# Kernel tuning notes

Measured on AMD Instinct MI355X. Metric: run time of the kernel, lower is better.

## Reference

```python
import jax, jax.numpy as jnp
import numpy as np

B, L, D_MODEL, EXPAND, HEADDIM, QK_DIM = 2, 512, 512, 2, 128, 16
D_INNER = EXPAND * D_MODEL            # 1024
NHEADS = D_INNER // HEADDIM           # 8
EPS = 1e-3
STD_DEV = 1.0 / np.sqrt(2 * L * QK_DIM)
TWO_PI = 2.0 * np.pi


def setup_inputs() -> dict:
    key = jax.random.key(0)
    kv, kq, kk = jax.random.split(key, 3)
    v = jax.random.normal(kv, (B, L, D_INNER), dtype=jnp.float32)
    q = jax.random.normal(kq, (B, L, NHEADS * QK_DIM), dtype=jnp.float32)
    k = jax.random.normal(kk, (B, L, NHEADS * QK_DIM), dtype=jnp.float32)
    return {"v": v, "q": q, "k": k}


def reference(v, q, k):
    b, l, dim = v.shape
    residual = v
    # b l (n h) -> b l n h
    vh = v.reshape(b, l, NHEADS, HEADDIM)
    # b l (n d) -> b n d l
    qh = q.reshape(b, l, NHEADS, QK_DIM).transpose(0, 2, 3, 1)
    kh = k.reshape(b, l, NHEADS, QK_DIM).transpose(0, 2, 3, 1)
    pos = jnp.arange(l, dtype=v.dtype)  # position indices
    c = jnp.asarray(TWO_PI * EPS, dtype=v.dtype)
    # q_matrix[b,n,d,t,l] = cos(c * q[b,n,d,t] * pos[l])
    q_mat = jnp.cos(c * qh[:, :, :, :, None] * pos)
    # k_matrix[b,n,d,l,t] = cos(c * k[b,n,d,t] * pos[l])
    k_mat = jnp.cos(c * kh[:, :, :, None, :] * pos[:, None])
    sym = (q_mat - k_mat).sum(axis=2)  # (b, n, t, l)
    out = jnp.einsum('bntl,blnh->btnh', sym, vh)
    out = jnp.asarray(STD_DEV, v.dtype) * out
    return out.reshape(b, l, dim) + residual
```

## Files before the change

kernel.cpp:

```cpp
#include <hip/hip_runtime.h>

#define L_SEQ   512
#define NHEADS_ 8
#define HEADDIM_ 128
#define QKD     16
#define DINNER  1024
#define EPS_F   1e-3f
#define STD_F   0.0078125f

#define KS_ROW  529

typedef __attribute__((ext_vector_type(8))) short  short8;
typedef __attribute__((ext_vector_type(4))) float  floatx4;
typedef __attribute__((ext_vector_type(2))) float  float2v;

__device__ __forceinline__ float cosrev(float rev) {
    float r = rev - floorf(rev);
    return __builtin_amdgcn_cosf(r);
}

__device__ __forceinline__ float two_cos_small(float a) {
    float x = a * a;
    return fmaf(fmaf(x, 129.8787876f, -39.4784176f), x, 2.0f);
}

__device__ __forceinline__ unsigned short f2bf_rne(float x) {
    union { float f; unsigned int u; } v;
    v.f = x;
    unsigned int r = v.u + 0x7fffu + ((v.u >> 16) & 1u);
    return (unsigned short)(r >> 16);
}

__device__ __forceinline__ short8 pack_bf16x8(const float* s) {
    union { int i[4]; short8 v; } u;
#pragma unroll
    for (int p = 0; p < 4; ++p)
        asm("v_cvt_pk_bf16_f32 %0, %1, %2"
            : "=v"(u.i[p]) : "v"(s[2 * p]), "v"(s[2 * p + 1]));
    return u.v;
}

__device__ __forceinline__ float tree8(const float2v* C) {
    float2v s = ((C[0] + C[1]) + (C[2] + C[3])) + ((C[4] + C[5]) + (C[6] + C[7]));
    return s.x + s.y;
}

__global__ __launch_bounds__(256) void vtrans_kernel(const float* __restrict__ v,
                                                     unsigned short* __restrict__ vt) {
    const int bid = blockIdx.x;
    const int tid = threadIdx.x;
    const int l0 = (bid & 7) * 64;
    const int h0 = ((bid >> 3) & 1) * 64;
    const int bn = bid >> 4;
    const int b = bn >> 3, n = bn & 7;
    __shared__ float tile[64][65];
    const float* vb = v + ((size_t)b * L_SEQ) * DINNER + n * HEADDIM_;
    float4 r[4];
#pragma unroll
    for (int i = 0; i < 4; ++i) {
        int f = i * 256 + tid;
        int hq = f & 15, ll = f >> 4;
        r[i] = *(const float4*)(vb + (size_t)(l0 + ll) * DINNER + (h0 + hq * 4));
    }
#pragma unroll
    for (int i = 0; i < 4; ++i) {
        int f = i * 256 + tid;
        int hq = f & 15, ll = f >> 4;
        tile[hq * 4 + 0][ll] = r[i].x;
        tile[hq * 4 + 1][ll] = r[i].y;
        tile[hq * 4 + 2][ll] = r[i].z;
        tile[hq * 4 + 3][ll] = r[i].w;
    }
    __syncthreads();
    unsigned short* vdst = vt + (size_t)bn * (64 * 128 * 8);
#pragma unroll
    for (int i = 0; i < 2; ++i) {
        int f = i * 256 + tid;
        int hh = f & 63;
        int lc = f >> 6;
        short8 pk;
#pragma unroll
        for (int j = 0; j < 8; ++j)
            pk[j] = (short)f2bf_rne(tile[hh][lc * 8 + j]);
        *(short8*)(vdst + ((size_t)((l0 >> 3) + lc) * 128 + (h0 + hh)) * 8) = pk;
    }
}

__global__ __launch_bounds__(256, 2) void vand_fused(const float* __restrict__ v,
                                                     const float* __restrict__ q,
                                                     const float* __restrict__ k,
                                                     const unsigned short* __restrict__ vt,
                                                     float* __restrict__ out) {
    const int tid  = threadIdx.x;
    const int w    = tid >> 6;
    const int lane = tid & 63;
    const int tl   = lane & 15;
    const int quad = lane >> 4;
    const int ttile = blockIdx.x;
    const int bn    = blockIdx.y;
    const int b = bn >> 3, n = bn & 7;
    const float t0f = (float)(ttile * 16);

    __shared__ float smem[16 * KS_ROW];
    float* ksl = smem;

    float4 kf[2][4];
#pragma unroll
    for (int rep = 0; rep < 2; ++rep) {
        const int l = w * 128 + rep * 64 + lane;
        const float* krow = k + ((size_t)(b * L_SEQ + l)) * (NHEADS_ * QKD) + n * QKD;
#pragma unroll
        for (int d4 = 0; d4 < 4; ++d4)
            kf[rep][d4] = *(const float4*)(krow + 4 * d4);
    }
    const int t = ttile * 16 + tl;
    const float* qrow = q + ((size_t)(b * L_SEQ + t)) * (NHEADS_ * QKD) + n * QKD;
    float4 qf[4];
#pragma unroll
    for (int d4 = 0; d4 < 4; ++d4)
        qf[d4] = *(const float4*)(qrow + 4 * d4);
    const float* vbase = v + ((size_t)b * L_SEQ) * DINNER + n * HEADDIM_;
    float4 vres[2];
    size_t gis[2];
#pragma unroll
    for (int i = 0; i < 2; ++i) {
        int g    = i * 256 + tid;
        int hb   = g & 31;
        int tloc = g >> 5;
        gis[i] = (size_t)(ttile * 16 + tloc) * DINNER + hb * 4;
        vres[i] = *(const float4*)(vbase + gis[i]);
    }

#pragma unroll
    for (int rep = 0; rep < 2; ++rep) {
        const int l = w * 128 + rep * 64 + lane;
        float kk[16];
#pragma unroll
        for (int d4 = 0; d4 < 4; ++d4) {
            kk[d4 * 4 + 0] = kf[rep][d4].x; kk[d4 * 4 + 1] = kf[rep][d4].y;
            kk[d4 * 4 + 2] = kf[rep][d4].z; kk[d4 * 4 + 3] = kf[rep][d4].w;
        }
        float2v M2[8], X[8], Y[8];
#pragma unroll
        for (int i = 0; i < 8; ++i) {
            float a0 = EPS_F * kk[2 * i], a1 = EPS_F * kk[2 * i + 1];
            M2[i].x = two_cos_small(a0);        M2[i].y = two_cos_small(a1);
            Y[i].x = cosrev(a0 * t0f);          Y[i].y = cosrev(a1 * t0f);
            X[i].x = cosrev(a0 * (t0f - 1.f));  X[i].y = cosrev(a1 * (t0f - 1.f));
        }
        int moff = (l >> 5) * 33 + (l & 31);
#pragma unroll 1
        for (int it = 0; it < 8; ++it) {
            ksl[moff] = tree8(Y);
#pragma unroll
            for (int i = 0; i < 8; ++i) X[i] = M2[i] * Y[i] - X[i];
            ksl[moff + KS_ROW] = tree8(X);
#pragma unroll
            for (int i = 0; i < 8; ++i) Y[i] = M2[i] * X[i] - Y[i];
            moff += 2 * KS_ROW;
        }
    }

    const int   l0  = w * 128 + quad * 32;
    const float l0f = (float)l0;
    float2v M2[8], X[8], Y[8];
#pragma unroll
    for (int d4 = 0; d4 < 4; ++d4) {
        float aa[4] = {EPS_F * qf[d4].x, EPS_F * qf[d4].y,
                       EPS_F * qf[d4].z, EPS_F * qf[d4].w};
#pragma unroll
        for (int e = 0; e < 2; ++e) {
            int i = d4 * 2 + e;
            float a0 = aa[2 * e], a1 = aa[2 * e + 1];
            M2[i].x = two_cos_small(a0);        M2[i].y = two_cos_small(a1);
            Y[i].x = cosrev(a0 * l0f);          Y[i].y = cosrev(a1 * l0f);
            X[i].x = cosrev(a0 * (l0f - 1.f));  X[i].y = cosrev(a1 * (l0f - 1.f));
        }
    }

    const unsigned short* vrow = vt + (size_t)bn * (64 * 128 * 8);
    const short* vp = (const short*)vrow + (w * 16 + quad * 4) * 1024 + tl * 8;
    int koff = tl * KS_ROW + (4 * w + quad) * 33;

    floatx4 acc[8] = {};

#pragma unroll 1
    for (int c = 0; c < 4; ++c) {
        short8 b0 = *(const short8*)(vp + 0 * 128);
        short8 b1 = *(const short8*)(vp + 1 * 128);
        short8 b2 = *(const short8*)(vp + 2 * 128);
        short8 b3 = *(const short8*)(vp + 3 * 128);
        short8 b4 = *(const short8*)(vp + 4 * 128);
        short8 b5 = *(const short8*)(vp + 5 * 128);
        short8 b6 = *(const short8*)(vp + 6 * 128);
        short8 b7 = *(const short8*)(vp + 7 * 128);
        float kv[8];
#pragma unroll
        for (int jj = 0; jj < 8; ++jj) kv[jj] = ksl[koff + jj];
        float ss[8];
#pragma unroll
        for (int p = 0; p < 4; ++p) {
            ss[2 * p] = tree8(Y) - kv[2 * p];
#pragma unroll
            for (int i = 0; i < 8; ++i) X[i] = M2[i] * Y[i] - X[i];
            ss[2 * p + 1] = tree8(X) - kv[2 * p + 1];
#pragma unroll
            for (int i = 0; i < 8; ++i) Y[i] = M2[i] * X[i] - Y[i];
        }
        const short8 af = pack_bf16x8(ss);
        acc[0] = __builtin_amdgcn_mfma_f32_16x16x32_bf16(af, b0, acc[0], 0, 0, 0);
        acc[1] = __builtin_amdgcn_mfma_f32_16x16x32_bf16(af, b1, acc[1], 0, 0, 0);
        acc[2] = __builtin_amdgcn_mfma_f32_16x16x32_bf16(af, b2, acc[2], 0, 0, 0);
        acc[3] = __builtin_amdgcn_mfma_f32_16x16x32_bf16(af, b3, acc[3], 0, 0, 0);
        acc[4] = __builtin_amdgcn_mfma_f32_16x16x32_bf16(af, b4, acc[4], 0, 0, 0);
        acc[5] = __builtin_amdgcn_mfma_f32_16x16x32_bf16(af, b5, acc[5], 0, 0, 0);
        acc[6] = __builtin_amdgcn_mfma_f32_16x16x32_bf16(af, b6, acc[6], 0, 0, 0);
        acc[7] = __builtin_amdgcn_mfma_f32_16x16x32_bf16(af, b7, acc[7], 0, 0, 0);
        vp += 1024;
        koff += 8;
    }

    __syncthreads();
    float (*red)[64][33] = (float (*)[64][33])smem;
#pragma unroll
    for (int ht = 0; ht < 8; ++ht)
#pragma unroll
        for (int r = 0; r < 4; ++r)
            red[w][lane][ht * 4 + r] = acc[ht][r];
    __syncthreads();

    float* obase = out + ((size_t)b * L_SEQ) * DINNER + n * HEADDIM_;
#pragma unroll
    for (int i = 0; i < 2; ++i) {
        int g    = i * 256 + tid;
        int hb   = g & 31;
        int tloc = g >> 5;
        int lidx0 = ((tloc >> 2) << 4) + ((hb & 3) << 2);
        int aidx  = ((hb >> 2) << 2) + (tloc & 3);
        float4 sum;
        float* sp = &sum.x;
#pragma unroll
        for (int e = 0; e < 4; ++e) {
            int lidx = lidx0 + e;
            sp[e] = (red[0][lidx][aidx] + red[1][lidx][aidx])
                  + (red[2][lidx][aidx] + red[3][lidx][aidx]);
        }
        float4 o;
        o.x = fmaf(STD_F, sum.x, vres[i].x);
        o.y = fmaf(STD_F, sum.y, vres[i].y);
        o.z = fmaf(STD_F, sum.z, vres[i].z);
        o.w = fmaf(STD_F, sum.w, vres[i].w);
        *(float4*)(obase + gis[i]) = o;
    }
}

extern "C" void kernel_launch(void* const* d_in, const int* in_sizes, int n_in,
                              void* d_out, int out_size, void* d_ws, size_t ws_size,
                              hipStream_t stream) {
    const float* v = (const float*)d_in[0];
    const float* q = (const float*)d_in[1];
    const float* k = (const float*)d_in[2];
    float* out = (float*)d_out;
    unsigned short* vt = (unsigned short*)d_ws;

    vtrans_kernel<<<dim3(256), 256, 0, stream>>>(v, vt);
    vand_fused<<<dim3(L_SEQ / 16, 16), 256, 0, stream>>>(v, q, k, vt, out);
}
```

Before: 75.59 us.

## Fuse V transpose and bf16 conversion into main kernel, drop pre-pass launch

Removes the separate vtrans_kernel that transposed V into a packed bf16 workspace. The fused kernel now reads fp32 V directly from global memory with strided scalar loads and converts each MFMA B-fragment to bf16 in registers. This saves one kernel launch and a round trip through the workspace. In exchange it issues many more uncoalesced 4-byte loads, and the V tiles are re-read and re-converted by every t-tile block.

```diff
diff --git a/kernel.cpp b/kernel.cpp
--- a/kernel.cpp
+++ b/kernel.cpp
@@ -24,13 +24,6 @@
     return fmaf(fmaf(x, 129.8787876f, -39.4784176f), x, 2.0f);
 }
 
-__device__ __forceinline__ unsigned short f2bf_rne(float x) {
-    union { float f; unsigned int u; } v;
-    v.f = x;
-    unsigned int r = v.u + 0x7fffu + ((v.u >> 16) & 1u);
-    return (unsigned short)(r >> 16);
-}
-
 __device__ __forceinline__ short8 pack_bf16x8(const float* s) {
     union { int i[4]; short8 v; } u;
 #pragma unroll
@@ -45,51 +38,9 @@
     return s.x + s.y;
 }
 
-__global__ __launch_bounds__(256) void vtrans_kernel(const float* __restrict__ v,
-                                                     unsigned short* __restrict__ vt) {
-    const int bid = blockIdx.x;
-    const int tid = threadIdx.x;
-    const int l0 = (bid & 7) * 64;
-    const int h0 = ((bid >> 3) & 1) * 64;
-    const int bn = bid >> 4;
-    const int b = bn >> 3, n = bn & 7;
-    __shared__ float tile[64][65];
-    const float* vb = v + ((size_t)b * L_SEQ) * DINNER + n * HEADDIM_;
-    float4 r[4];
-#pragma unroll
-    for (int i = 0; i < 4; ++i) {
-        int f = i * 256 + tid;
-        int hq = f & 15, ll = f >> 4;
-        r[i] = *(const float4*)(vb + (size_t)(l0 + ll) * DINNER + (h0 + hq * 4));
-    }
-#pragma unroll
-    for (int i = 0; i < 4; ++i) {
-        int f = i * 256 + tid;
-        int hq = f & 15, ll = f >> 4;
-        tile[hq * 4 + 0][ll] = r[i].x;
-        tile[hq * 4 + 1][ll] = r[i].y;
-        tile[hq * 4 + 2][ll] = r[i].z;
-        tile[hq * 4 + 3][ll] = r[i].w;
-    }
-    __syncthreads();
-    unsigned short* vdst = vt + (size_t)bn * (64 * 128 * 8);
-#pragma unroll
-    for (int i = 0; i < 2; ++i) {
-        int f = i * 256 + tid;
-        int hh = f & 63;
-        int lc = f >> 6;
-        short8 pk;
-#pragma unroll
-        for (int j = 0; j < 8; ++j)
-            pk[j] = (short)f2bf_rne(tile[hh][lc * 8 + j]);
-        *(short8*)(vdst + ((size_t)((l0 >> 3) + lc) * 128 + (h0 + hh)) * 8) = pk;
-    }
-}
-
 __global__ __launch_bounds__(256, 2) void vand_fused(const float* __restrict__ v,
                                                      const float* __restrict__ q,
                                                      const float* __restrict__ k,
-                                                     const unsigned short* __restrict__ vt,
                                                      float* __restrict__ out) {
     const int tid  = threadIdx.x;
     const int w    = tid >> 6;
@@ -178,22 +129,13 @@
         }
     }
 
-    const unsigned short* vrow = vt + (size_t)bn * (64 * 128 * 8);
-    const short* vp = (const short*)vrow + (w * 16 + quad * 4) * 1024 + tl * 8;
+    const float* vbp = vbase + (size_t)l0 * DINNER + tl;
     int koff = tl * KS_ROW + (4 * w + quad) * 33;
 
     floatx4 acc[8] = {};
 
 #pragma unroll 1
     for (int c = 0; c < 4; ++c) {
-        short8 b0 = *(const short8*)(vp + 0 * 128);
-        short8 b1 = *(const short8*)(vp + 1 * 128);
-        short8 b2 = *(const short8*)(vp + 2 * 128);
-        short8 b3 = *(const short8*)(vp + 3 * 128);
-        short8 b4 = *(const short8*)(vp + 4 * 128);
-        short8 b5 = *(const short8*)(vp + 5 * 128);
-        short8 b6 = *(const short8*)(vp + 6 * 128);
-        short8 b7 = *(const short8*)(vp + 7 * 128);
         float kv[8];
 #pragma unroll
         for (int jj = 0; jj < 8; ++jj) kv[jj] = ksl[koff + jj];
@@ -208,15 +150,17 @@
             for (int i = 0; i < 8; ++i) Y[i] = M2[i] * X[i] - Y[i];
         }
         const short8 af = pack_bf16x8(ss);
-        acc[0] = __builtin_amdgcn_mfma_f32_16x16x32_bf16(af, b0, acc[0], 0, 0, 0);
-        acc[1] = __builtin_amdgcn_mfma_f32_16x16x32_bf16(af, b1, acc[1], 0, 0, 0);
-        acc[2] = __builtin_amdgcn_mfma_f32_16x16x32_bf16(af, b2, acc[2], 0, 0, 0);
-        acc[3] = __builtin_amdgcn_mfma_f32_16x16x32_bf16(af, b3, acc[3], 0, 0, 0);
-        acc[4] = __builtin_amdgcn_mfma_f32_16x16x32_bf16(af, b4, acc[4], 0, 0, 0);
-        acc[5] = __builtin_amdgcn_mfma_f32_16x16x32_bf16(af, b5, acc[5], 0, 0, 0);
-        acc[6] = __builtin_amdgcn_mfma_f32_16x16x32_bf16(af, b6, acc[6], 0, 0, 0);
-        acc[7] = __builtin_amdgcn_mfma_f32_16x16x32_bf16(af, b7, acc[7], 0, 0, 0);
-        vp += 1024;
+
+#pragma unroll
+        for (int ht = 0; ht < 8; ++ht) {
+            float fv[8];
+#pragma unroll
+            for (int jj = 0; jj < 8; ++jj)
+                fv[jj] = vbp[(size_t)jj * DINNER + ht * 16];
+            const short8 bfr = pack_bf16x8(fv);
+            acc[ht] = __builtin_amdgcn_mfma_f32_16x16x32_bf16(af, bfr, acc[ht], 0, 0, 0);
+        }
+        vbp += 8 * DINNER;
         koff += 8;
     }
 
@@ -261,8 +205,7 @@
     const float* q = (const float*)d_in[1];
     const float* k = (const float*)d_in[2];
     float* out = (float*)d_out;
-    unsigned short* vt = (unsigned short*)d_ws;
-
-    vtrans_kernel<<<dim3(256), 256, 0, stream>>>(v, vt);
-    vand_fused<<<dim3(L_SEQ / 16, 16), 256, 0, stream>>>(v, q, k, vt, out);
-}
+    (void)d_ws; (void)ws_size;
+
+    vand_fused<<<dim3(L_SEQ / 16, 16), 256, 0, stream>>>(v, q, k, out);
+}
```

After: 93.12 us. 23.2% more time.
